# Optimization experiments

Measured on AMD Instinct MI355X. Metric: run time of the kernel, lower is better.

Reference implementation:

```python
import jax, jax.numpy as jnp
import numpy as np
import math

T, P, ITERS, H = 6, 8, 2, 8          # nr_types, num_proto, iters, n_head
D, F = 512, 1024                      # dim_proto, feature_dim (hidden_dim==D)
L = T * ITERS                         # 12 cross-attention layers


def _ln(x, g=None, b=None, eps=1e-5):
    m = x.mean(-1, keepdims=True)
    v = x.var(-1, keepdims=True)
    y = (x - m) * jax.lax.rsqrt(v + eps)
    if g is not None:
        y = y * g + b
    return y


def _forward(x_batch, batch_mask, node_type, pm_W, pm_b, pm_g, pm_bn,
             proto_logsigma, rand_mul, Wq, bq, Wk, bk, Wv, bv, Wo, bo,
             ag, ab, Wm1, bm1, lg, lb, Wm2, bm2, pg, pb):
    B, N, _ = x_batch.shape
    dt = x_batch.dtype
    bm = batch_mask.astype(dt)                                   # [B,N]
    onehot = jax.nn.one_hot(node_type, T, dtype=dt)              # [B,N,T]
    valid = bm * jnp.any(x_batch != 0, axis=-1).astype(dt)       # [B,N]
    mbt = onehot * valid[:, :, None]                             # [B,N,T]
    sums = jnp.einsum('bnt,bnf->btf', mbt, x_batch)              # per-(batch,type) sum
    cnt = mbt.sum(1)                                             # [B,T]
    fallback = x_batch.sum(1) / bm.sum(1, keepdims=True)         # [B,F]
    proto_mu = jnp.where(cnt[..., None] > 0,
                         sums / jnp.maximum(cnt, 1.0)[..., None],
                         fallback[:, None, :])                   # [B,T,F]

    # proto_mlp: Linear + LayerNorm + GELU (dropout = eval/identity)
    mu = jax.nn.gelu(_ln(proto_mu @ pm_W + pm_b, pm_g, pm_bn), approximate=False)  # [B,T,D]
    all_proto = mu[:, :, None, :] + jnp.exp(proto_logsigma)[None] * rand_mul[None]  # [B,T,P,D]

    dh = D // H
    scale = 1.0 / math.sqrt(dh)
    keymask = bm[:, None, None, :] == 0                          # [B,1,1,N]

    def layer(q, i):
        resid = q                                                 # [B,P,D]
        k = _ln((x_batch @ Wk[i] + bk[i]).reshape(B, N, H, dh))   # QK-LayerNorm (no affine)
        v = (x_batch @ Wv[i] + bv[i]).reshape(B, N, H, dh)
        qh = _ln((q @ Wq[i] + bq[i]).reshape(B, P, H, dh))
        dots = jnp.einsum('bkhd,bnhd->bkhn', qh, k) * scale       # [B,P,H,N]
        dots = jnp.where(keymask, -jnp.inf, dots)
        attn = jax.nn.softmax(dots, axis=-1)
        upd = jnp.einsum('bnhd,bkhn->bkhd', v, attn).reshape(B, P, D)
        upd = upd @ Wo[i] + bo[i]
        q = resid + _ln(upd, ag[i], ab[i])
        h = jax.nn.gelu(_ln(q @ Wm1[i] + bm1[i], lg[i], lb[i]), approximate=False)
        h = h @ Wm2[i] + bm2[i]
        return q + _ln(h, pg[i], pb[i])

    outs = []
    c = 0
    for i in range(T):
        p = all_proto[:, i]
        for _ in range(ITERS):
            p = layer(p, c)
            c += 1
        outs.append(p)
    prototypes = jnp.stack(outs, axis=1)                          # [B,T,P,D]
    return prototypes, proto_mu


def setup_inputs() -> dict:
    key = jax.random.key(0)
    ks = jax.random.split(key, 40)
    B, N = 4, 4096
    sc = 0.02

    def rn(i, shape, s=sc):
        return jax.random.normal(ks[i], shape, jnp.float32) * s

    inp = {
        'x_batch': jax.random.normal(ks[0], (B, N, F), jnp.float32),
        'batch_mask': jax.random.randint(ks[1], (B, N), 0, 2, jnp.int32),
        'node_type': jax.random.randint(ks[2], (B, N), 0, T, jnp.int32),
        'pm_W': rn(3, (F, D)), 'pm_b': jnp.zeros((D,)),
        'pm_g': jnp.ones((D,)), 'pm_bn': jnp.zeros((D,)),
        'proto_logsigma': rn(4, (T, 1, D), 0.05),
        'rand_mul': jax.random.normal(ks[5], (T, P, D), jnp.float32),
        'Wq': rn(6, (L, D, D)), 'bq': jnp.zeros((L, D)),
        'Wk': rn(7, (L, F, D)), 'bk': jnp.zeros((L, D)),
        'Wv': rn(8, (L, F, D)), 'bv': jnp.zeros((L, D)),
        'Wo': rn(9, (L, D, D)), 'bo': jnp.zeros((L, D)),
        'ag': jnp.ones((L, D)), 'ab': jnp.zeros((L, D)),
        'Wm1': rn(10, (L, D, D)), 'bm1': jnp.zeros((L, D)),
        'lg': jnp.ones((L, D)), 'lb': jnp.zeros((L, D)),
        'Wm2': rn(11, (L, D, D)), 'bm2': jnp.zeros((L, D)),
        'pg': jnp.ones((L, D)), 'pb': jnp.zeros((L, D)),
    }
    return inp


def reference(x_batch, batch_mask, node_type, pm_W, pm_b, pm_g, pm_bn,
              proto_logsigma, rand_mul, Wq, bq, Wk, bk, Wv, bv, Wo, bo,
              ag, ab, Wm1, bm1, lg, lb, Wm2, bm2, pg, pb):
    return _forward(x_batch, batch_mask, node_type, pm_W, pm_b, pm_g, pm_bn,
                    proto_logsigma, rand_mul, Wq, bq, Wk, bk, Wv, bv, Wo, bo,
                    ag, ab, Wm1, bm1, lg, lb, Wm2, bm2, pg, pb)
```

## Files before the change

### kernel.cpp

```cpp
#include <hip/hip_runtime.h>
#include <hip/hip_bf16.h>
#include <stdint.h>

#define TT 6
#define PP 8
#define HH 8
#define DD 512
#define FF 1024
#define DH 64
#define NB 4
#define NN 4096
#define LL 12
#define NCH 16
#define CHK 256
#define NXB 128

typedef __attribute__((ext_vector_type(8))) short short8v;
typedef __attribute__((ext_vector_type(4))) float f32x4;
typedef __attribute__((ext_vector_type(4))) unsigned short u16x4;
typedef __attribute__((ext_vector_type(8))) unsigned short u16x8;
typedef unsigned short u16;

__device__ __forceinline__ float bf2f(u16 u){
  union { unsigned int i; float f; } x; x.i = ((unsigned int)u) << 16; return x.f;
}
__device__ __forceinline__ u16 f2bf(float f){
  union { float f; unsigned int i; } x; x.f = f;
  unsigned int r = x.i + 0x7fffu + ((x.i >> 16) & 1u);
  return (u16)(r >> 16);
}
__device__ __forceinline__ float wave_sum(float x){
  #pragma unroll
  for (int o = 32; o > 0; o >>= 1) x += __shfl_xor(x, o);
  return x;
}
__device__ __forceinline__ float ldf(const void* p, size_t i, int f32){
  float v;
  if (f32) v = ((const float*)p)[i];
  else     v = bf2f(((const u16*)p)[i]);
  return v;
}
__device__ __forceinline__ float gemv_vec(const float* __restrict__ xs,
    const void* __restrict__ W, size_t wbase, int ktot, int wf32,
    float* __restrict__ red, int tid){
  int g = tid & 63, sl = tid >> 6;
  int kpw = ktot >> 3;
  float a[8] = {0,0,0,0,0,0,0,0};
  if (wf32){
    const float* Wp = (const float*)W + wbase + (size_t)(sl*kpw)*DD + g*8;
    #pragma unroll 4
    for (int i = 0; i < kpw; ++i){
      float xv = xs[sl*kpw + i];
      f32x4 lo = *(const f32x4*)(Wp + (size_t)i*DD);
      f32x4 hi = *(const f32x4*)(Wp + (size_t)i*DD + 4);
      a[0]+=xv*lo.x; a[1]+=xv*lo.y; a[2]+=xv*lo.z; a[3]+=xv*lo.w;
      a[4]+=xv*hi.x; a[5]+=xv*hi.y; a[6]+=xv*hi.z; a[7]+=xv*hi.w;
    }
  } else {
    const u16* Wp = (const u16*)W + wbase + (size_t)(sl*kpw)*DD + g*8;
    #pragma unroll 4
    for (int i = 0; i < kpw; ++i){
      float xv = xs[sl*kpw + i];
      u16x8 w8 = *(const u16x8*)(Wp + (size_t)i*DD);
      #pragma unroll
      for (int j = 0; j < 8; ++j) a[j] += xv * bf2f(w8[j]);
    }
  }
  #pragma unroll
  for (int j = 0; j < 8; ++j) red[sl*512 + g*8 + j] = a[j];
  __syncthreads();
  float y = 0;
  #pragma unroll
  for (int s2 = 0; s2 < 8; ++s2) y += red[s2*512 + tid];
  return y;
}
__device__ __forceinline__ void glds16(const void* g, void* l){
#if __has_builtin(__builtin_amdgcn_global_load_lds)
  __builtin_amdgcn_global_load_lds(
      (const __attribute__((address_space(1))) void*)g,
      (__attribute__((address_space(3))) void*)l, 16, 0, 0);
#else
  *(u16x8*)l = *(const u16x8*)g;
#endif
}
__device__ __forceinline__ void tail_gemm8(f32x4 acc[4], const u16* __restrict__ Bp,
    const u16* As, int l15, int q4, int n0w){
  #pragma unroll
  for (int ni = 0; ni < 4; ++ni){ f32x4 z = {0,0,0,0}; acc[ni] = z; }
  #pragma unroll 2
  for (int k0 = 0; k0 < 512; k0 += 32){
    short8v bf[4], af;
    #pragma unroll
    for (int ni = 0; ni < 4; ++ni)
      bf[ni] = *(const short8v*)(Bp + (size_t)(n0w + ni*16 + l15)*DD + k0 + q4*8);
    af = *(const short8v*)(As + l15*520 + k0 + q4*8);
    #pragma unroll
    for (int ni = 0; ni < 4; ++ni)
      acc[ni] = __builtin_amdgcn_mfma_f32_16x16x32_bf16(af, bf[ni], acc[ni], 0, 0, 0);
  }
}
__device__ __forceinline__ void row_ln8(const f32x4 acc[4],
    float* red1, float* red2, int w, int l15, int q4,
    float mv[4], float rv[4]){
  float s1[4], s2[4];
  #pragma unroll
  for (int r = 0; r < 4; ++r){
    float a0=acc[0][r], a1=acc[1][r], a2=acc[2][r], a3=acc[3][r];
    s1[r] = (a0+a1)+(a2+a3);
    s2[r] = (a0*a0+a1*a1)+(a2*a2+a3*a3);
  }
  #pragma unroll
  for (int o = 1; o < 16; o <<= 1)
    #pragma unroll
    for (int r = 0; r < 4; ++r){
      s1[r] += __shfl_xor(s1[r], o);
      s2[r] += __shfl_xor(s2[r], o);
    }
  if (l15 == 0){
    #pragma unroll
    for (int r = 0; r < 4; ++r){
      int row = q4*4 + r;
      red1[row*8 + w] = s1[r];
      red2[row*8 + w] = s2[r];
    }
  }
  __syncthreads();
  #pragma unroll
  for (int r = 0; r < 4; ++r){
    int row = q4*4 + r;
    float S1 = 0, S2 = 0;
    #pragma unroll
    for (int j = 0; j < 8; ++j){ S1 += red1[row*8+j]; S2 += red2[row*8+j]; }
    float m = S1 * (1.f/DD);
    float var = S2 * (1.f/DD) - m*m;
    mv[r] = m;
    rv[r] = rsqrtf(var + 1e-5f);
  }
  __syncthreads();
}

__global__ void k_detect(const void* __restrict__ X, int* __restrict__ flag){
  int tid = threadIdx.x;
  const u16* u = (const u16*)X;
  int bad = 0;
  for (int i = tid; i < 8192; i += 256){
    int ex = (u[i] >> 7) & 0xFF;
    if (ex >= 0x90) bad = 1;
  }
  __shared__ int s;
  if (tid == 0) s = 0;
  __syncthreads();
  if (bad) s = 1;
  __syncthreads();
  if (tid == 0) *flag = s;
}

__global__ void k_cvt2(const void* __restrict__ s0, u16* __restrict__ d0, int n0q,
                       const void* __restrict__ s1, u16* __restrict__ d1,
                       const int* __restrict__ flagp){
  int f32 = *flagp;
  size_t q = (size_t)blockIdx.x*256 + threadIdx.x;
  const void* s; u16* d; size_t i;
  if (q < (size_t)n0q){ s = s0; d = d0; i = q*4; }
  else                { s = s1; d = d1; i = (q - n0q)*4; }
  if (f32){
    f32x4 v = *(const f32x4*)((const float*)s + i);
    u16x4 o; o.x=f2bf(v.x); o.y=f2bf(v.y); o.z=f2bf(v.z); o.w=f2bf(v.w);
    *(u16x4*)(d+i) = o;
  } else {
    *(u16x4*)(d+i) = *(const u16x4*)((const u16*)s + i);
  }
}

__global__ void k_xcv(const void* __restrict__ X, u16* __restrict__ Xb,
                      const int* __restrict__ bm, const int* __restrict__ ntype,
                      float* __restrict__ Pcol, float* __restrict__ Ptot,
                      float* __restrict__ cnt, float* __restrict__ bmsum,
                      const int* __restrict__ flagp){
  int f32 = *flagp;
  int b = blockIdx.y, blk = blockIdx.x;
  int n0 = blk * 32;
  int tid = threadIdx.x;
  int f0 = tid * 4;
  __shared__ int sflag[32];
  __shared__ float scnt[TT+1];
  if (tid < 32) sflag[tid] = 0;
  if (tid < TT+1) scnt[tid] = 0.f;
  __syncthreads();
  float acc[TT][4] = {};
  float tot[4] = {0,0,0,0};
  for (int i = 0; i < 32; ++i){
    int n = n0 + i;
    size_t idx = (size_t)(b*NN+n)*FF + f0;
    u16x4 xb;
    bool a;
    if (f32){
      f32x4 v = *(const f32x4*)((const float*)X + idx);
      xb.x=f2bf(v.x); xb.y=f2bf(v.y); xb.z=f2bf(v.z); xb.w=f2bf(v.w);
      a = (v.x!=0.f)||(v.y!=0.f)||(v.z!=0.f)||(v.w!=0.f);
    } else {
      xb = *(const u16x4*)((const u16*)X + idx);
      a = (bf2f(xb.x)!=0.f)||(bf2f(xb.y)!=0.f)||(bf2f(xb.z)!=0.f)||(bf2f(xb.w)!=0.f);
    }
    *(u16x4*)(Xb+idx) = xb;
    if (a) sflag[i] = 1;
    float vbm = (bm[b*NN+n] != 0) ? 1.f : 0.f;
    int ty = ntype[b*NN+n];
    #pragma unroll
    for (int j = 0; j < 4; ++j){
      float xv = bf2f(xb[j]);
      tot[j] += xv;
      float xvv = xv * vbm;
      #pragma unroll
      for (int t = 0; t < TT; ++t) acc[t][j] += (ty==t) ? xvv : 0.f;
    }
  }
  __syncthreads();
  if (tid < 32){
    int n = n0 + tid;
    if (bm[b*NN+n] != 0){
      if (sflag[tid]) atomicAdd(&scnt[ntype[b*NN+n]], 1.f);
      atomicAdd(&scnt[TT], 1.f);
    }
  }
  size_t pbase = (size_t)blk*NB + b;
  #pragma unroll
  for (int t = 0; t < TT; ++t){
    f32x4 v = {acc[t][0], acc[t][1], acc[t][2], acc[t][3]};
    *(f32x4*)&Pcol[(pbase*TT + t)*FF + f0] = v;
  }
  {
    f32x4 v = {tot[0], tot[1], tot[2], tot[3]};
    *(f32x4*)&Ptot[pbase*FF + f0] = v;
  }
  __syncthreads();
  if (tid < TT) atomicAdd(&cnt[b*TT + tid], scnt[tid]);
  if (tid == TT) atomicAdd(&bmsum[b], scnt[TT]);
}

__global__ void k_compact(const int* __restrict__ bm, int* __restrict__ nidx,
                          int* __restrict__ cntc){
  int b = blockIdx.x, tid = threadIdx.x;
  __shared__ int csum[256];
  __shared__ int pref[257];
  int base = b*NN + tid*16;
  int f[16]; int loc = 0;
  #pragma unroll
  for (int i = 0; i < 16; ++i){ f[i] = (bm[base+i] != 0); loc += f[i]; }
  csum[tid] = loc;
  __syncthreads();
  if (tid == 0){
    pref[0] = 0;
    for (int j = 0; j < 256; ++j) pref[j+1] = pref[j] + csum[j];
  }
  __syncthreads();
  int off = b*NN + pref[tid];
  #pragma unroll
  for (int i = 0; i < 16; ++i){ if (f[i]) nidx[off++] = tid*16 + i; }
  if (tid == 0) cntc[b] = pref[256];
}

__global__ void k_wbfT(const void* __restrict__ Wq, const void* __restrict__ Wo,
                       const void* __restrict__ Wm1, const void* __restrict__ Wm2,
                       u16* __restrict__ Wt, const int* __restrict__ flagp){
  int f32 = *flagp;
  int z = blockIdx.z;
  int fam = z / LL;
  const void* src = (fam==0) ? Wq : (fam==1) ? Wo : (fam==2) ? Wm1 : Wm2;
  size_t sbase = (size_t)(z % LL) * DD * DD;
  __shared__ u16 tile[32][33];
  int d0 = blockIdx.x*32, k0 = blockIdx.y*32;
  int tx = threadIdx.x, ty = threadIdx.y;
  #pragma unroll
  for (int i = 0; i < 4; ++i){
    size_t idx = sbase + (size_t)(k0 + ty + i*8)*DD + d0 + tx;
    u16 v;
    if (f32) v = f2bf(((const float*)src)[idx]);
    else     v = ((const u16*)src)[idx];
    tile[ty + i*8][tx] = v;
  }
  __syncthreads();
  #pragma unroll
  for (int i = 0; i < 4; ++i)
    Wt[((size_t)z*DD + d0 + ty + i*8)*DD + k0 + tx] = tile[tx][ty + i*8];
}

__global__ void __launch_bounds__(512) k_mu(const float* __restrict__ Pcol,
   const float* __restrict__ Ptot, const float* __restrict__ cnt,
   const float* __restrict__ bmsum,
   const void* __restrict__ pmWx, const void* __restrict__ pmb,
   const void* __restrict__ pmg, const void* __restrict__ pmbn,
   const void* __restrict__ lsig, const void* __restrict__ rmul,
   float* __restrict__ qstate, void* __restrict__ dout, int wmode,
   const int* __restrict__ flagp){
  int f32 = *flagp;
  int wf32 = wmode ? f32 : 0;
  const size_t OFFP = (size_t)NB*TT*PP*DD;
  int bt = blockIdx.x; int b = bt/TT, t = bt%TT;
  int d = threadIdx.x;
  __shared__ float xs[FF];
  __shared__ float red[4096];
  __shared__ float r1[8], r2[8];
  float cv = cnt[bt];
  float inv = 1.f / fmaxf(cv, 1.f);
  float fbinv = 1.f / bmsum[b];
  #pragma unroll
  for (int h = 0; h < 2; ++h){
    int f = d + h*512;
    float S = 0.f, T = 0.f;
    for (int blk = 0; blk < NXB; ++blk){
      size_t pbase = (size_t)blk*NB + b;
      S += Pcol[(pbase*TT + t)*FF + f];
      T += Ptot[pbase*FF + f];
    }
    float pm = (cv > 0.f) ? S * inv : T * fbinv;
    xs[f] = pm;
    if (f32) ((float*)dout)[OFFP + (size_t)bt*FF + f] = pm;
    else     ((u16*)dout)[OFFP + (size_t)bt*FF + f] = f2bf(pm);
  }
  __syncthreads();
  float acc = ldf(pmb, d, f32) + gemv_vec(xs, pmWx, 0, FF, wf32, red, d);
  int lane = d & 63, wid = d >> 6;
  float s1 = wave_sum(acc), s2 = wave_sum(acc*acc);
  if (lane==0){ r1[wid]=s1; r2[wid]=s2; }
  __syncthreads();
  float m=0, qq=0;
  #pragma unroll
  for (int i=0;i<8;++i){ m+=r1[i]; qq+=r2[i]; }
  m *= (1.f/DD); float var = qq*(1.f/DD) - m*m;
  float y = (acc - m) * rsqrtf(var + 1e-5f) * ldf(pmg, d, f32) + ldf(pmbn, d, f32);
  float mu = 0.5f * y * (1.f + erff(y * 0.70710678118654752f));
  #pragma unroll
  for (int p = 0; p < PP; ++p){
    float rv = ldf(rmul, (size_t)(t*PP+p)*DD + d, f32);
    float ls = ldf(lsig, (size_t)t*DD + d, f32);
    qstate[(((size_t)(b*TT+t))*PP + p)*DD + d] = mu + expf(ls) * rv;
  }
}

__global__ void k_transpose(const void* __restrict__ Wk, const void* __restrict__ Wv,
                            u16* __restrict__ TK, u16* __restrict__ TV,
                            int tlo, int s, const int* __restrict__ flagp){
  int f32 = *flagp;
  int ti = blockIdx.z >> 1, kv = blockIdx.z & 1;
  int c = 2*(tlo+ti)+s;
  size_t eoff = (size_t)c*FF*DD;
  const void* W = kv ? Wv : Wk;
  u16* T = (kv ? TV : TK) + (size_t)ti*FF*DD;
  __shared__ u16 tile[32][33];
  int n0 = blockIdx.x * 32, k0 = blockIdx.y * 32;
  int tx = threadIdx.x, ty = threadIdx.y;
  #pragma unroll
  for (int i = 0; i < 4; ++i){
    size_t idx = eoff + (size_t)(k0 + ty + i*8)*DD + n0 + tx;
    u16 v;
    if (f32) v = f2bf(((const float*)W)[idx]);
    else     v = ((const u16*)W)[idx];
    tile[ty + i*8][tx] = v;
  }
  __syncthreads();
  #pragma unroll
  for (int i = 0; i < 4; ++i)
    T[(size_t)(n0 + ty + i*8)*FF + k0 + tx] = tile[tx][ty + i*8];
}

__global__ void __launch_bounds__(512) k_kvgemm(const u16* __restrict__ Xb,
    const u16* __restrict__ TK, const u16* __restrict__ TV,
    const void* __restrict__ bk, const void* __restrict__ bv,
    u16* __restrict__ Kb, u16* __restrict__ Vb,
    const int* __restrict__ nidx, const int* __restrict__ cntc,
    int tlo, int s, int nt, const int* __restrict__ flagp){
  int f32 = *flagp;
  int orig = blockIdx.x;
  int x = orig & 7, r = orig >> 3;
  int bx = r / nt, pr = r - bx*nt;
  int pairg = x*nt + pr;
  int by = pairg & 3; int kvti = pairg >> 2; int kv = kvti & 1; int ti = kvti >> 1;
  int b = bx >> 4, jt = bx & 15;
  int cnt = cntc[b];
  if (jt*256 >= cnt) return;
  int c = 2*(tlo+ti)+s;
  size_t boff = (size_t)c*DD;
  const u16* WT = (kv ? TV : TK) + (size_t)ti*FF*DD;
  const void* bias = kv ? bv : bk;
  u16* out = (kv ? Vb : Kb) + (size_t)ti*((size_t)NB*NN*DD);
  int n0 = by*128;
  __shared__ __align__(16) char LDS[3*24576];
  int tid = threadIdx.x, wid = tid >> 6, lane = tid & 63;
  int wr = wid >> 1, wcn = wid & 1;
  const u16* gp0; const u16* gp1; const u16* gp2;
  int lo0, lo1, lo2;
  {
    const u16* gps[3]; int los[3];
    #pragma unroll
    for (int i = 0; i < 3; ++i){
      int e = tid + i*512;
      if (e < 1024){
        int row = e>>2, sp = e&3;
        int ssrc = sp ^ (((row>>3)&1)<<1);
        int cl = jt*256 + row; if (cl >= cnt) cl = cnt-1;
        int grow = nidx[b*NN + cl];
        gps[i] = Xb + ((size_t)b*NN + grow)*FF + ssrc*8;
        los[i] = e*16;
      } else {
        int e2 = e - 1024;
        int row = e2>>2, sp = e2&3;
        int ssrc = sp ^ (((row>>3)&1)<<1);
        gps[i] = WT + (size_t)(n0 + row)*FF + ssrc*8;
        los[i] = 16384 + e2*16;
      }
    }
    gp0=gps[0]; gp1=gps[1]; gp2=gps[2];
    lo0=los[0]; lo1=los[1]; lo2=los[2];
  }
#define STAGE(T) { char* bb_ = LDS + ((T)%3)*24576; \
  glds16(gp0 + (T)*32, bb_ + lo0); glds16(gp1 + (T)*32, bb_ + lo1); \
  glds16(gp2 + (T)*32, bb_ + lo2); }
  int ke = (lane>>4) ^ (((lane>>3)&1)<<1);
  int arow[4], brow[4];
  #pragma unroll
  for (int mi = 0; mi < 4; ++mi)
    arow[mi] = (wr*64 + mi*16 + (lane&15))*64 + ke*16;
  #pragma unroll
  for (int ni = 0; ni < 4; ++ni)
    brow[ni] = 16384 + (wcn*64 + ni*16 + (lane&15))*64 + ke*16;
  f32x4 acc[4][4] = {};
  STAGE(0);
  STAGE(1);
  asm volatile("s_waitcnt vmcnt(3)" ::: "memory");
  __builtin_amdgcn_sched_barrier(0);
  __builtin_amdgcn_s_barrier();
  __builtin_amdgcn_sched_barrier(0);
  #pragma unroll
  for (int t = 0; t < 32; ++t){
    const char* Bbuf = LDS + (t%3)*24576;
    short8v af[4], bf[4];
    #pragma unroll
    for (int mi = 0; mi < 4; ++mi)
      af[mi] = *(const short8v*)(Bbuf + arow[mi]);
    #pragma unroll
    for (int ni = 0; ni < 4; ++ni)
      bf[ni] = *(const short8v*)(Bbuf + brow[ni]);
    if (t + 2 <= 31) STAGE(t+2);
    __builtin_amdgcn_s_setprio(1);
    #pragma unroll
    for (int mi = 0; mi < 4; ++mi)
      #pragma unroll
      for (int ni = 0; ni < 4; ++ni)
        acc[mi][ni] = __builtin_amdgcn_mfma_f32_16x16x32_bf16(af[mi], bf[ni], acc[mi][ni], 0, 0, 0);
    __builtin_amdgcn_s_setprio(0);
    if (t < 30)       asm volatile("s_waitcnt vmcnt(3)" ::: "memory");
    else if (t == 30) asm volatile("s_waitcnt vmcnt(0)" ::: "memory");
    __builtin_amdgcn_sched_barrier(0);
    if (t < 31){
      __builtin_amdgcn_s_barrier();
      __builtin_amdgcn_sched_barrier(0);
    }
  }
#undef STAGE
  #pragma unroll
  for (int mi = 0; mi < 4; ++mi){
    #pragma unroll
    for (int ni = 0; ni < 4; ++ni){
      int col = n0 + wcn*64 + ni*16 + (lane & 15);
      int h = col >> 6, dh = col & 63;
      float bvf = ldf(bias, boff + col, f32);
      #pragma unroll
      for (int r2 = 0; r2 < 4; ++r2){
        int row = jt*256 + wr*64 + mi*16 + (lane>>4)*4 + r2;
        out[(((size_t)(b*HH + h))*NN + row)*DH + dh] = f2bf(acc[mi][ni][r2] + bvf);
      }
    }
  }
}

__global__ void __launch_bounds__(512) k_qproj(const float* __restrict__ qstate,
      const void* __restrict__ Wq, const void* __restrict__ bq,
      float* __restrict__ qh, int tlo, int s, int wmode,
      const int* __restrict__ flagp){
  int f32 = *flagp;
  int wf32 = wmode ? f32 : 0;
  int z = blockIdx.x; int ti = z >> 5, rr = z & 31;
  int b = rr >> 3, p = rr & 7;
  int t = tlo + ti, c = 2*t + s;
  size_t woff = (size_t)c*DD*DD, boff = (size_t)c*DD;
  int d = threadIdx.x;
  __shared__ float xs[DD];
  __shared__ float red[4096];
  const float* xrow = qstate + (((size_t)(b*TT+t))*PP + p)*DD;
  xs[d] = xrow[d];
  __syncthreads();
  float acc = ldf(bq, boff + d, f32) + gemv_vec(xs, Wq, woff, DD, wf32, red, d);
  float s1 = wave_sum(acc) * (1.f/DH);
  float s2 = wave_sum(acc*acc) * (1.f/DH);
  float var = s2 - s1*s1;
  qh[(size_t)z*DD + d] = (acc - s1) * rsqrtf(var + 1e-5f);
}

__global__ void __launch_bounds__(512) k_attnA(const u16* __restrict__ Kb,
     const u16* __restrict__ Vb, const float* __restrict__ qh,
     const int* __restrict__ cntc, float* __restrict__ Opart, float* __restrict__ lpart){
  int ic = blockIdx.x, bh = blockIdx.y, ti = blockIdx.z;
  int b = bh >> 3, h = bh & 7;
  int cnt = cntc[b];
  if (ic*CHK >= cnt) return;
  int tid = threadIdx.x, p8 = tid >> 6, ln = tid & 63;
  int r8 = ln >> 3, g = ln & 7;
  __shared__ __align__(16) char KV[32768];
  __shared__ float qs[PP*DH];
  __shared__ float qsum[PP];
  __shared__ float e_lds[CHK*9];
  int rem = cnt - ic*CHK;
  float qv = qh[((size_t)(ti*32 + b*PP + p8))*DD + h*DH + ln];
  size_t tioff = (size_t)ti*((size_t)NB*NN*DD);
  const u16* Kbase = Kb + tioff + ((size_t)(b*HH + h)*NN + (size_t)ic*CHK)*DH;
  const u16* Vbase = Vb + tioff + ((size_t)(b*HH + h)*NN + (size_t)ic*CHK)*DH;
  #pragma unroll
  for (int i = 0; i < 4; ++i){
    int e = tid + i*512;
    int row = e >> 3, sp = e & 7;
    int ss = sp ^ (row & 7);
    int rr = row < rem ? row : rem-1;
    glds16(Vbase + (size_t)rr*DH + ss*8, (char*)KV + e*16);
  }
  qs[p8*DH + ln] = qv;
  {
    float sQ = wave_sum(qv);
    if (ln == 0) qsum[p8] = sQ;
  }
  asm volatile("s_waitcnt lgkmcnt(0)" ::: "memory");
  __builtin_amdgcn_sched_barrier(0);
  __builtin_amdgcn_s_barrier();
  __builtin_amdgcn_sched_barrier(0);
  #pragma unroll
  for (int it = 0; it < CHK/64; ++it){
    int nl = it*64 + p8*8 + r8;
    int rr8 = nl < rem ? nl : rem-1;
    u16x8 kv8 = *(const u16x8*)(Kbase + (size_t)rr8*DH + g*8);
    float kf[8];
    #pragma unroll
    for (int e = 0; e < 8; ++e) kf[e] = bf2f(kv8[e]);
    float sm = 0, sq = 0;
    #pragma unroll
    for (int e = 0; e < 8; ++e){ sm += kf[e]; sq += kf[e]*kf[e]; }
    #pragma unroll
    for (int o = 1; o < 8; o <<= 1){
      sm += __shfl_xor(sm, o);
      sq += __shfl_xor(sq, o);
    }
    sm *= (1.f/DH); sq = sq*(1.f/DH) - sm*sm;
    float inv = rsqrtf(sq + 1e-5f);
    float ap[8];
    #pragma unroll
    for (int p = 0; p < 8; ++p){
      f32x4 qa = *(const f32x4*)&qs[p*DH + g*8];
      f32x4 qb = *(const f32x4*)&qs[p*DH + g*8 + 4];
      ap[p] = kf[0]*qa.x + kf[1]*qa.y + kf[2]*qa.z + kf[3]*qa.w
            + kf[4]*qb.x + kf[5]*qb.y + kf[6]*qb.z + kf[7]*qb.w;
    }
    #pragma unroll
    for (int o = 1; o < 8; o <<= 1){
      #pragma unroll
      for (int p = 0; p < 8; ++p) ap[p] += __shfl_xor(ap[p], o);
    }
    float dg = (g==0)?ap[0]:(g==1)?ap[1]:(g==2)?ap[2]:(g==3)?ap[3]
             : (g==4)?ap[4]:(g==5)?ap[5]:(g==6)?ap[6]:ap[7];
    float sv = (dg - sm*qsum[g]) * inv * 0.125f;
    e_lds[nl*9 + g] = (nl < rem) ? __expf(sv) : 0.f;
  }
  __syncthreads();
  {
    float lp = 0;
    #pragma unroll
    for (int j = 0; j < CHK/64; ++j) lp += e_lds[(ln + j*64)*9 + p8];
    lp = wave_sum(lp);
    if (ln == 0) lpart[((size_t)(ti*32+bh)*NCH + ic)*PP + p8] = lp;
  }
  {
    float a0=0,a1=0,a2=0,a3=0,a4=0,a5=0,a6=0,a7=0;
    int vseg = (r8 ^ g) * 16;
    #pragma unroll 4
    for (int m = 0; m < CHK/8; ++m){
      float e = e_lds[(g + m*8)*9 + p8];
      u16x8 vv = *(const u16x8*)((const char*)KV + (g + m*8)*128 + vseg);
      a0 += e*bf2f(vv[0]); a1 += e*bf2f(vv[1]);
      a2 += e*bf2f(vv[2]); a3 += e*bf2f(vv[3]);
      a4 += e*bf2f(vv[4]); a5 += e*bf2f(vv[5]);
      a6 += e*bf2f(vv[6]); a7 += e*bf2f(vv[7]);
    }
    #pragma unroll
    for (int o = 1; o < 8; o <<= 1){
      a0 += __shfl_xor(a0, o); a1 += __shfl_xor(a1, o);
      a2 += __shfl_xor(a2, o); a3 += __shfl_xor(a3, o);
      a4 += __shfl_xor(a4, o); a5 += __shfl_xor(a5, o);
      a6 += __shfl_xor(a6, o); a7 += __shfl_xor(a7, o);
    }
    if (g == 0){
      float* op = Opart + ((size_t)(ti*32+bh)*NCH + ic)*512 + p8*64 + r8*8;
      f32x4 lo = {a0,a1,a2,a3}, hi = {a4,a5,a6,a7};
      *(f32x4*)op = lo;
      *((f32x4*)op + 1) = hi;
    }
  }
}

__global__ void __launch_bounds__(512) k_tailm(
    const float* __restrict__ Opart, const float* __restrict__ lpart,
    const int* __restrict__ cntc,
    float* __restrict__ qstate, float* __restrict__ qh,
    const u16* __restrict__ Wt,
    const void* __restrict__ bo, const void* __restrict__ ag, const void* __restrict__ ab,
    const void* __restrict__ bm1, const void* __restrict__ lg, const void* __restrict__ lb,
    const void* __restrict__ bm2, const void* __restrict__ pg, const void* __restrict__ pb,
    const void* __restrict__ bq, void* __restrict__ dout,
    int tlo, int s, int nt, const int* __restrict__ flagp){
  int f32 = *flagp;
  int ti = blockIdx.x & 7, b = blockIdx.x >> 3;
  if (ti >= nt) return;
  int t = tlo + ti, c = 2*t + s;
  int tid = threadIdx.x;
  int w = tid >> 6, lane = tid & 63, q4 = lane >> 4, l15 = lane & 15;
  int n0w = w*64;
  size_t boff = (size_t)c*DD;
  const size_t famSz = (size_t)LL*DD*DD;
  __shared__ u16 As[16*520];
  __shared__ float red1[128], red2[128];
  __shared__ float lval[64];
  int nch = (cntc[b] + CHK - 1) / CHK;
  for (int i = tid; i < 16*520; i += 512) As[i] = 0;
  if (tid < 64){
    int p = tid >> 3, hh = tid & 7;
    float l = 0;
    for (int ic = 0; ic < nch; ++ic)
      l += lpart[((size_t)(ti*32 + b*8 + hh)*NCH + ic)*PP + p];
    lval[tid] = 1.f / l;
  }
  __syncthreads();
  {
    int hh = tid >> 6, dd = tid & 63;
    #pragma unroll
    for (int p = 0; p < 8; ++p){
      float o = 0;
      for (int ic = 0; ic < nch; ++ic)
        o += Opart[((size_t)(ti*32 + b*8 + hh)*NCH + ic)*512 + p*64 + dd];
      As[p*520 + hh*64 + dd] = f2bf(o * lval[p*8 + hh]);
    }
  }
  __syncthreads();
  f32x4 acc[4], q2[4];
  float mv[4], rv[4];
  size_t qoffb = ((size_t)(b*TT+t))*PP*DD;
  {
    const u16* Bp = Wt + famSz + (size_t)c*DD*DD;
    tail_gemm8(acc, Bp, As, l15, q4, n0w);
    #pragma unroll
    for (int ni = 0; ni < 4; ++ni){
      float bv = ldf(bo, boff + n0w + ni*16 + l15, f32);
      #pragma unroll
      for (int r = 0; r < 4; ++r) acc[ni][r] += bv;
    }
    row_ln8(acc, red1, red2, w, l15, q4, mv, rv);
    #pragma unroll
    for (int ni = 0; ni < 4; ++ni){
      int col = n0w + ni*16 + l15;
      float gm = ldf(ag, boff + col, f32), bt = ldf(ab, boff + col, f32);
      #pragma unroll
      for (int r = 0; r < 4; ++r){
        int row = q4*4 + r;
        float y = (acc[ni][r] - mv[r])*rv[r]*gm + bt;
        float res = (q4 < 2) ? qstate[qoffb + (size_t)row*DD + col] : 0.f;
        q2[ni][r] = res + y;
      }
    }
    if (q4 < 2){
      #pragma unroll
      for (int r = 0; r < 4; ++r){
        int row = q4*4 + r;
        #pragma unroll
        for (int ni = 0; ni < 4; ++ni)
          As[row*520 + n0w + ni*16 + l15] = f2bf(q2[ni][r]);
      }
    }
  }
  __syncthreads();
  {
    const u16* Bp = Wt + 2*famSz + (size_t)c*DD*DD;
    tail_gemm8(acc, Bp, As, l15, q4, n0w);
    #pragma unroll
    for (int ni = 0; ni < 4; ++ni){
      float bv = ldf(bm1, boff + n0w + ni*16 + l15, f32);
      #pragma unroll
      for (int r = 0; r < 4; ++r) acc[ni][r] += bv;
    }
    row_ln8(acc, red1, red2, w, l15, q4, mv, rv);
    #pragma unroll
    for (int ni = 0; ni < 4; ++ni){
      int col = n0w + ni*16 + l15;
      float gm = ldf(lg, boff + col, f32), bt = ldf(lb, boff + col, f32);
      #pragma unroll
      for (int r = 0; r < 4; ++r){
        int row = q4*4 + r;
        float y = (acc[ni][r] - mv[r])*rv[r]*gm + bt;
        y = 0.5f*y*(1.f + erff(y*0.70710678118654752f));
        if (q4 < 2) As[row*520 + col] = f2bf(y);
      }
    }
  }
  __syncthreads();
  {
    const u16* Bp = Wt + 3*famSz + (size_t)c*DD*DD;
    tail_gemm8(acc, Bp, As, l15, q4, n0w);
    #pragma unroll
    for (int ni = 0; ni < 4; ++ni){
      float bv = ldf(bm2, boff + n0w + ni*16 + l15, f32);
      #pragma unroll
      for (int r = 0; r < 4; ++r) acc[ni][r] += bv;
    }
    row_ln8(acc, red1, red2, w, l15, q4, mv, rv);
    #pragma unroll
    for (int ni = 0; ni < 4; ++ni){
      int col = n0w + ni*16 + l15;
      float gm = ldf(pg, boff + col, f32), bt = ldf(pb, boff + col, f32);
      #pragma unroll
      for (int r = 0; r < 4; ++r){
        int row = q4*4 + r;
        float outv = q2[ni][r] + (acc[ni][r] - mv[r])*rv[r]*gm + bt;
        if (q4 < 2){
          qstate[qoffb + (size_t)row*DD + col] = outv;
          if (s == 0) As[row*520 + col] = f2bf(outv);
          else {
            if (f32) ((float*)dout)[qoffb + (size_t)row*DD + col] = outv;
            else     ((u16*)dout)[qoffb + (size_t)row*DD + col] = f2bf(outv);
          }
        }
      }
    }
  }
  if (s == 0){
    __syncthreads();
    const u16* Bp = Wt + (size_t)(c+1)*DD*DD;
    tail_gemm8(acc, Bp, As, l15, q4, n0w);
    #pragma unroll
    for (int ni = 0; ni < 4; ++ni){
      float bv = ldf(bq, (size_t)(c+1)*DD + n0w + ni*16 + l15, f32);
      #pragma unroll
      for (int r = 0; r < 4; ++r) acc[ni][r] += bv;
    }
    float s1[4], s2[4];
    #pragma unroll
    for (int r = 0; r < 4; ++r){
      float a0=acc[0][r], a1=acc[1][r], a2=acc[2][r], a3=acc[3][r];
      s1[r] = (a0+a1)+(a2+a3);
      s2[r] = (a0*a0+a1*a1)+(a2*a2+a3*a3);
    }
    #pragma unroll
    for (int o = 1; o < 16; o <<= 1)
      #pragma unroll
      for (int r = 0; r < 4; ++r){
        s1[r] += __shfl_xor(s1[r], o);
        s2[r] += __shfl_xor(s2[r], o);
      }
    if (q4 < 2){
      #pragma unroll
      for (int r = 0; r < 4; ++r){
        int row = q4*4 + r;
        float m = s1[r] * (1.f/DH);
        float var = s2[r] * (1.f/DH) - m*m;
        float ri = rsqrtf(var + 1e-5f);
        #pragma unroll
        for (int ni = 0; ni < 4; ++ni){
          int col = n0w + ni*16 + l15;
          qh[((size_t)(ti*32 + b*8 + row))*DD + col] = (acc[ni][r] - m)*ri;
        }
      }
    }
  }
}

__global__ void __launch_bounds__(512) k_tail(
    const float* __restrict__ Opart, const float* __restrict__ lpart,
    const int* __restrict__ cntc,
    float* __restrict__ qstate, float* __restrict__ qh,
    const void* __restrict__ Wo_, const void* __restrict__ Wm1_,
    const void* __restrict__ Wm2_, const void* __restrict__ Wq_,
    const void* __restrict__ bo, const void* __restrict__ ag, const void* __restrict__ ab,
    const void* __restrict__ bm1, const void* __restrict__ lg, const void* __restrict__ lb,
    const void* __restrict__ bm2, const void* __restrict__ pg, const void* __restrict__ pb,
    const void* __restrict__ bq,
    int tlo, int s, int wmode, const int* __restrict__ flagp){
  int f32 = *flagp;
  int wf32 = wmode ? f32 : 0;
  int z = blockIdx.x; int ti = z >> 5, rr = z & 31;
  int b = rr >> 3, p = rr & 7;
  int t = tlo + ti, c = 2*t + s;
  int d = threadIdx.x;
  int h = d >> 6, dd = d & 63;
  int lane = d & 63, wid = d >> 6;
  size_t qoff = (((size_t)(b*TT+t))*PP + p)*DD;
  size_t boff = (size_t)c*DD;
  size_t w0 = (size_t)c*DD*DD;
  __shared__ float xs[DD];
  __shared__ float red[4096];
  __shared__ float r1[8], r2[8];
  int nch = (cntc[b] + CHK - 1) / CHK;
  float o = 0, l = 0;
  for (int ic = 0; ic < nch; ++ic){
    o += Opart[((size_t)(ti*32 + b*8 + h)*NCH + ic)*512 + p*64 + dd];
    l += lpart[((size_t)(ti*32 + b*8 + h)*NCH + ic)*PP + p];
  }
  float upd = o / l;
  xs[d] = upd;
  __syncthreads();
  float acc = ldf(bo, boff + d, f32) + gemv_vec(xs, Wo_, w0, DD, wf32, red, d);
  {
    float s1 = wave_sum(acc), s2 = wave_sum(acc*acc);
    if (lane == 0){ r1[wid] = s1; r2[wid] = s2; }
  }
  __syncthreads();
  float m = 0, qv = 0;
  #pragma unroll
  for (int i = 0; i < 8; ++i){ m += r1[i]; qv += r2[i]; }
  m *= (1.f/DD); float var = qv*(1.f/DD) - m*m;
  float y = (acc - m)*rsqrtf(var + 1e-5f)*ldf(ag, boff+d, f32) + ldf(ab, boff+d, f32);
  float q2 = qstate[qoff + d] + y;
  __syncthreads();
  xs[d] = q2;
  __syncthreads();
  float acc2 = ldf(bm1, boff + d, f32) + gemv_vec(xs, Wm1_, w0, DD, wf32, red, d);
  {
    float s1 = wave_sum(acc2), s2 = wave_sum(acc2*acc2);
    if (lane == 0){ r1[wid] = s1; r2[wid] = s2; }
  }
  __syncthreads();
  m = 0; qv = 0;
  #pragma unroll
  for (int i = 0; i < 8; ++i){ m += r1[i]; qv += r2[i]; }
  m *= (1.f/DD); var = qv*(1.f/DD) - m*m;
  float y2 = (acc2 - m)*rsqrtf(var + 1e-5f)*ldf(lg, boff+d, f32) + ldf(lb, boff+d, f32);
  y2 = 0.5f*y2*(1.f + erff(y2*0.70710678118654752f));
  __syncthreads();
  xs[d] = y2;
  __syncthreads();
  float acc3 = ldf(bm2, boff + d, f32) + gemv_vec(xs, Wm2_, w0, DD, wf32, red, d);
  {
    float s1 = wave_sum(acc3), s2 = wave_sum(acc3*acc3);
    if (lane == 0){ r1[wid] = s1; r2[wid] = s2; }
  }
  __syncthreads();
  m = 0; qv = 0;
  #pragma unroll
  for (int i = 0; i < 8; ++i){ m += r1[i]; qv += r2[i]; }
  m *= (1.f/DD); var = qv*(1.f/DD) - m*m;
  float y3 = (acc3 - m)*rsqrtf(var + 1e-5f)*ldf(pg, boff+d, f32) + ldf(pb, boff+d, f32);
  float outv = q2 + y3;
  qstate[qoff + d] = outv;
  if (s == 0){
    __syncthreads();
    xs[d] = outv;
    __syncthreads();
    size_t w1 = (size_t)(c+1)*DD*DD;
    float accq = ldf(bq, (size_t)(c+1)*DD + d, f32) + gemv_vec(xs, Wq_, w1, DD, wf32, red, d);
    float t1 = wave_sum(accq) * (1.f/DH);
    float t2 = wave_sum(accq*accq) * (1.f/DH);
    float var2 = t2 - t1*t1;
    qh[(size_t)z*DD + d] = (accq - t1) * rsqrtf(var2 + 1e-5f);
  }
}

__global__ void k_out(const float* __restrict__ qstate, void* __restrict__ dout,
                      const int* __restrict__ flagp){
  int f32 = *flagp;
  int i = blockIdx.x*256 + threadIdx.x;
  if (f32) ((float*)dout)[i] = qstate[i];
  else     ((u16*)dout)[i] = f2bf(qstate[i]);
}

extern "C" void kernel_launch(void* const* d_in, const int* in_sizes, int n_in,
                              void* d_out, int out_size, void* d_ws, size_t ws_size,
                              hipStream_t stream){
  (void)in_sizes; (void)n_in; (void)out_size;
  const void* X   = d_in[0];
  const int* bm    = (const int*)d_in[1];
  const int* ntype = (const int*)d_in[2];
  const void* pmW = d_in[3];  const void* pmb = d_in[4];
  const void* pmg = d_in[5];  const void* pmbn= d_in[6];
  const void* lsig= d_in[7];  const void* rmul= d_in[8];
  const void* Wq  = d_in[9];  const void* bq  = d_in[10];
  const void* Wk  = d_in[11]; const void* bk  = d_in[12];
  const void* Wv  = d_in[13]; const void* bv  = d_in[14];
  const void* Wo  = d_in[15]; const void* bo  = d_in[16];
  const void* ag  = d_in[17]; const void* ab  = d_in[18];
  const void* Wm1 = d_in[19]; const void* bm1 = d_in[20];
  const void* lg  = d_in[21]; const void* lb  = d_in[22];
  const void* Wm2 = d_in[23]; const void* bm2 = d_in[24];
  const void* pg  = d_in[25]; const void* pb  = d_in[26];

  char* ws = (char*)d_ws;
  int*   flagp    = (int*)(ws + 0);
  float* cnt      = (float*)(ws + 256);
  float* bmsum    = (float*)(ws + 512);
  float* qstate   = (float*)(ws + 279296);
  int*   cntc     = (int*)(ws + 672512);
  int*   nidx     = (int*)(ws + 672768);

  size_t off = 738304;
  auto take = [&](size_t bytes)->char*{
    char* p = ws + off; off = (off + bytes + 255) & ~(size_t)255; return p;
  };
  u16* Xbf = (u16*)take((size_t)NB*NN*FF*2);

  const size_t perT = (size_t)65536
                    + 16384
                    + 1048576
                    + 2*1048576
                    + 2*16777216;
  const size_t wtBytes = (size_t)4*LL*DD*DD*2;
  const size_t pmwbB   = (size_t)FF*DD*2;
  const size_t wqbB    = (size_t)LL*DD*DD*2;
  size_t base = off;

  int nt = 1;
  if      (ws_size >= base + 6*perT + 65536) nt = 6;
  else if (ws_size >= base + 3*perT + 65536) nt = 3;
  else if (ws_size >= base + 2*perT + 65536) nt = 2;

  float* qh    = (float*)take((size_t)nt*65536);
  float* lpart = (float*)take((size_t)nt*16384);
  float* Opart = (float*)take((size_t)nt*1048576);
  u16*   WkT   = (u16*)take((size_t)nt*1048576);
  u16*   WvT   = (u16*)take((size_t)nt*1048576);
  u16*   Kb    = (u16*)take((size_t)nt*16777216);
  u16*   Vb    = (u16*)take((size_t)nt*16777216);

  int useWt = (ws_size >= off + wtBytes + 65536) ? 1 : 0;
  u16* Wt = useWt ? (u16*)take(wtBytes) : nullptr;
  int useCvt = (ws_size >= off + pmwbB + wqbB + 65536) ? 1 : 0;
  u16* pmWb = useCvt ? (u16*)take(pmwbB) : nullptr;
  u16* Wqb  = useCvt ? (u16*)take(wqbB)  : nullptr;

  const void* WqG = useCvt ? (const void*)Wqb : Wq;
  int wmode = useCvt ? 0 : 1;

  float* Pcol = (float*)Kb;
  float* Ptot = (float*)((char*)Kb + (size_t)NXB*NB*TT*FF*4);

  hipMemsetAsync(ws + 256, 0, 512, stream);
  k_detect<<<1, 256, 0, stream>>>(X, flagp);
  k_compact<<<NB, 256, 0, stream>>>(bm, nidx, cntc);
  if (useWt)
    k_wbfT<<<dim3(16, 16, 4*LL), dim3(32, 8), 0, stream>>>(Wq, Wo, Wm1, Wm2, Wt, flagp);
  if (useCvt){
    const int n0q = (FF*DD)/4;
    const int nblk = (FF*DD + LL*DD*DD)/4/256;
    k_cvt2<<<nblk, 256, 0, stream>>>(pmW, pmWb, n0q, Wq, Wqb, flagp);
  }
  k_xcv<<<dim3(NXB, NB), 256, 0, stream>>>(X, Xbf, bm, ntype, Pcol, Ptot,
                                           cnt, bmsum, flagp);
  if (useCvt)
    k_mu<<<NB*TT, 512, 0, stream>>>(Pcol, Ptot, cnt, bmsum,
        pmWb, pmb, pmg, pmbn, lsig, rmul, qstate, d_out, 0, flagp);
  else
    k_mu<<<NB*TT, 512, 0, stream>>>(Pcol, Ptot, cnt, bmsum,
        pmW, pmb, pmg, pmbn, lsig, rmul, qstate, d_out, 1, flagp);

  for (int tlo = 0; tlo < TT; tlo += nt){
    for (int s = 0; s < 2; ++s){
      k_transpose<<<dim3(16, 32, 2*nt), dim3(32, 8), 0, stream>>>(
          Wk, Wv, WkT, WvT, tlo, s, flagp);
      k_kvgemm<<<64*8*nt, 512, 0, stream>>>(
          Xbf, WkT, WvT, bk, bv, Kb, Vb, nidx, cntc, tlo, s, nt, flagp);
      if (s == 0)
        k_qproj<<<nt*32, 512, 0, stream>>>(qstate, WqG, bq, qh, tlo, 0, wmode, flagp);
      k_attnA<<<dim3(NCH, 32, nt), 512, 0, stream>>>(Kb, Vb, qh, cntc, Opart, lpart);
      if (useWt)
        k_tailm<<<32, 512, 0, stream>>>(Opart, lpart, cntc, qstate, qh, Wt,
            bo, ag, ab, bm1, lg, lb, bm2, pg, pb, bq, d_out, tlo, s, nt, flagp);
      else
        k_tail<<<nt*32, 512, 0, stream>>>(Opart, lpart, cntc, qstate, qh,
            Wo, Wm1, Wm2, Wq, bo, ag, ab, bm1, lg, lb, bm2, pg, pb, bq,
            tlo, s, 1, flagp);
    }
  }
  if (!useWt)
    k_out<<<NB*TT*PP*DD/256, 256, 0, stream>>>(qstate, d_out, flagp);
}
```

Baseline: 625.9 us.

## Split partial-sum fold into separate kernel and coalesce K/V GEMM epilogue stores via LDS

```diff
diff --git a/kernel.cpp b/kernel.cpp
--- a/kernel.cpp
+++ b/kernel.cpp
@@ -238,6 +238,26 @@
   if (tid == TT) atomicAdd(&bmsum[b], scnt[TT]);
 }
 
+__global__ void k_fold(const float* __restrict__ Pcol, const float* __restrict__ Ptot,
+                       float* __restrict__ colsums, float* __restrict__ coltotal){
+  int fb = blockIdx.x;
+  int bt = blockIdx.y;
+  int b = bt / TT, t = bt % TT;
+  int f = fb*256 + threadIdx.x;
+  float S = 0.f;
+  #pragma unroll 4
+  for (int blk = 0; blk < NXB; ++blk)
+    S += Pcol[(((size_t)blk*NB + b)*TT + t)*FF + f];
+  colsums[(size_t)bt*FF + f] = S;
+  if (t == 0){
+    float T = 0.f;
+    #pragma unroll 4
+    for (int blk = 0; blk < NXB; ++blk)
+      T += Ptot[((size_t)blk*NB + b)*FF + f];
+    coltotal[b*FF + f] = T;
+  }
+}
+
 __global__ void k_compact(const int* __restrict__ bm, int* __restrict__ nidx,
                           int* __restrict__ cntc){
   int b = blockIdx.x, tid = threadIdx.x;
@@ -285,8 +305,8 @@
     Wt[((size_t)z*DD + d0 + ty + i*8)*DD + k0 + tx] = tile[tx][ty + i*8];
 }
 
-__global__ void __launch_bounds__(512) k_mu(const float* __restrict__ Pcol,
-   const float* __restrict__ Ptot, const float* __restrict__ cnt,
+__global__ void __launch_bounds__(512) k_mu(const float* __restrict__ colsums,
+   const float* __restrict__ coltotal, const float* __restrict__ cnt,
    const float* __restrict__ bmsum,
    const void* __restrict__ pmWx, const void* __restrict__ pmb,
    const void* __restrict__ pmg, const void* __restrict__ pmbn,
@@ -307,13 +327,8 @@
   #pragma unroll
   for (int h = 0; h < 2; ++h){
     int f = d + h*512;
-    float S = 0.f, T = 0.f;
-    for (int blk = 0; blk < NXB; ++blk){
-      size_t pbase = (size_t)blk*NB + b;
-      S += Pcol[(pbase*TT + t)*FF + f];
-      T += Ptot[pbase*FF + f];
-    }
-    float pm = (cv > 0.f) ? S * inv : T * fbinv;
+    float pm = (cv > 0.f) ? colsums[(size_t)bt*FF + f] * inv
+                          : coltotal[b*FF + f] * fbinv;
     xs[f] = pm;
     if (f32) ((float*)dout)[OFFP + (size_t)bt*FF + f] = pm;
     else     ((u16*)dout)[OFFP + (size_t)bt*FF + f] = f2bf(pm);
@@ -458,18 +473,32 @@
     }
   }
 #undef STAGE
+  __syncthreads();
+  u16* Lw = (u16*)LDS + wid*(64*68);
+  int q4 = lane >> 4, l15 = lane & 15;
   #pragma unroll
   for (int mi = 0; mi < 4; ++mi){
     #pragma unroll
     for (int ni = 0; ni < 4; ++ni){
-      int col = n0 + wcn*64 + ni*16 + (lane & 15);
-      int h = col >> 6, dh = col & 63;
+      int col = n0 + wcn*64 + ni*16 + l15;
       float bvf = ldf(bias, boff + col, f32);
       #pragma unroll
       for (int r2 = 0; r2 < 4; ++r2){
-        int row = jt*256 + wr*64 + mi*16 + (lane>>4)*4 + r2;
-        out[(((size_t)(b*HH + h))*NN + row)*DH + dh] = f2bf(acc[mi][ni][r2] + bvf);
+        int rl = mi*16 + q4*4 + r2;
+        Lw[rl*68 + ni*16 + l15] = f2bf(acc[mi][ni][r2] + bvf);
       }
+    }
+  }
+  {
+    int row0g = jt*256 + wr*64;
+    int colg0 = n0 + wcn*64 + (lane&7)*8;
+    int hg = colg0 >> 6, dhg = colg0 & 63;
+    #pragma unroll
+    for (int ps = 0; ps < 8; ++ps){
+      int rl = ps*8 + (lane>>3);
+      u16x8 v = *(u16x8*)&Lw[rl*68 + (lane&7)*8];
+      int row = row0g + rl;
+      *(u16x8*)&out[(((size_t)(b*HH + hg))*NN + row)*DH + dhg] = v;
     }
   }
 }
@@ -899,6 +928,8 @@
   int*   flagp    = (int*)(ws + 0);
   float* cnt      = (float*)(ws + 256);
   float* bmsum    = (float*)(ws + 512);
+  float* colsums  = (float*)(ws + 768);
+  float* coltotal = (float*)(ws + 99072);
   float* qstate   = (float*)(ws + 279296);
   int*   cntc     = (int*)(ws + 672512);
   int*   nidx     = (int*)(ws + 672768);
@@ -956,11 +987,12 @@
   }
   k_xcv<<<dim3(NXB, NB), 256, 0, stream>>>(X, Xbf, bm, ntype, Pcol, Ptot,
                                            cnt, bmsum, flagp);
+  k_fold<<<dim3(4, NB*TT), 256, 0, stream>>>(Pcol, Ptot, colsums, coltotal);
   if (useCvt)
-    k_mu<<<NB*TT, 512, 0, stream>>>(Pcol, Ptot, cnt, bmsum,
+    k_mu<<<NB*TT, 512, 0, stream>>>(colsums, coltotal, cnt, bmsum,
         pmWb, pmb, pmg, pmbn, lsig, rmul, qstate, d_out, 0, flagp);
   else
-    k_mu<<<NB*TT, 512, 0, stream>>>(Pcol, Ptot, cnt, bmsum,
+    k_mu<<<NB*TT, 512, 0, stream>>>(colsums, coltotal, cnt, bmsum,
         pmW, pmb, pmg, pmbn, lsig, rmul, qstate, d_out, 1, flagp);
 
   for (int tlo = 0; tlo < TT; tlo += nt){
```

Measured after the change: 676.6 us. +8.1%, slower.
